# Kernel tuning notes

Hardware: AMD Instinct MI355X
Metric: run time of the kernel (lower is better)

The kernel has to match this reference:

```python
import jax, jax.numpy as jnp
import numpy as np
from jax import lax

ALPHA = 0.85
C1 = 0.01 ** 2
C2 = 0.03 ** 2


def _avg_pool3(x):
    # F.avg_pool2d(x, 3, 1, 1) with count_include_pad=True: zero-pad, divide by 9.
    s = lax.reduce_window(x, jnp.array(0.0, x.dtype), lax.add,
                          (1, 1, 3, 3), (1, 1, 1, 1),
                          [(0, 0), (0, 0), (1, 1), (1, 1)])
    return s / jnp.array(9.0, x.dtype)


def _ssim(x, y):
    mu_x = _avg_pool3(x)
    mu_y = _avg_pool3(y)
    sigma_x = jnp.clip(_avg_pool3(x * x) - mu_x * mu_x, 0.0, None)
    sigma_y = jnp.clip(_avg_pool3(y * y) - mu_y * mu_y, 0.0, None)
    sigma_xy = _avg_pool3(x * y) - mu_x * mu_y
    ssim_n = (2.0 * mu_x * mu_y + C1) * (2.0 * sigma_xy + C2)
    ssim_d = (mu_x * mu_x + mu_y * mu_y + C1) * (sigma_x + sigma_y + C2)
    return jnp.clip((1.0 - ssim_n / ssim_d) / 2.0, 0.0, 1.0)


def _warp_right(right_img, disp):
    # grid_sample(bilinear, border, align_corners=True) where y maps identically
    # to its own row -> a 1D horizontal bilinear gather at x_sample = x - disp.
    B, C, H, W = right_img.shape
    x_base = jnp.arange(W, dtype=disp.dtype).reshape(1, 1, 1, W)
    x_sample = x_base - disp                      # [B,1,H,W]
    xs = jnp.clip(x_sample, 0.0, W - 1.0)         # border padding
    x0 = jnp.floor(xs)
    w = xs - x0                                   # frac weight
    i0 = x0.astype(jnp.int32)
    i1 = jnp.minimum(i0 + 1, W - 1)
    i0b = jnp.broadcast_to(i0, (B, C, H, W))
    i1b = jnp.broadcast_to(i1, (B, C, H, W))
    g0 = jnp.take_along_axis(right_img, i0b, axis=3)
    g1 = jnp.take_along_axis(right_img, i1b, axis=3)
    warped = (1.0 - w) * g0 + w * g1              # w broadcasts over C
    valid = ((x_sample > 0) & (x_sample < W - 1)).astype(disp.dtype)
    return warped, valid


def setup_inputs() -> dict:
    key = jax.random.key(0)
    k1, k2, k3 = jax.random.split(key, 3)
    B, H, W = 8, 720, 1280
    disp = jax.random.normal(k1, (B, 1, H, W), dtype=jnp.float32)
    left_img = jax.random.uniform(k2, (B, 3, H, W), dtype=jnp.float32)
    right_img = jax.random.uniform(k3, (B, 3, H, W), dtype=jnp.float32)
    return {"disp": disp, "left_img": left_img, "right_img": right_img}


def reference(disp, left_img, right_img):
    right_warped, valid = _warp_right(right_img, disp)
    l1_err = jnp.mean(jnp.abs(left_img - right_warped), axis=1, keepdims=True)
    ssim_err = jnp.mean(_ssim(left_img, right_warped), axis=1, keepdims=True)
    photo_err = ALPHA * ssim_err + (1.0 - ALPHA) * l1_err
    n_valid = jnp.maximum(jnp.sum(valid), 1.0)
    return jnp.sum(photo_err * valid) / n_valid
```

## Files before the change

### kernel.cpp

```cpp
#include <hip/hip_runtime.h>


#define P_ALPHA 0.85f
#define P_C1 1e-4f
#define P_C2 9e-4f

constexpr int COLS = 62;
constexpr int RPW  = 18;
constexpr int WAVES = 4;

__global__ __launch_bounds__(256)
void photo_loss_kernel(const float* __restrict__ disp,
                       const float* __restrict__ left,
                       const float* __restrict__ right,
                       float* __restrict__ acc,
                       int H, int W)
{
    __shared__ float redpv[WAVES];
    __shared__ float redv[WAVES];

    const int tid  = threadIdx.x;
    const int lane = tid & 63;
    const int w    = tid >> 6;
    const int b    = blockIdx.z;
    const int col  = blockIdx.x * COLS + lane - 1;
    const int rowStart = (blockIdx.y * WAVES + w) * RPW;

    const int planeHW = H * W;
    const float* __restrict__ dispb = disp  + b * planeHW;
    const float* __restrict__ L0 = left  + (b * 3 + 0) * planeHW;
    const float* __restrict__ L1 = left  + (b * 3 + 1) * planeHW;
    const float* __restrict__ L2 = left  + (b * 3 + 2) * planeHW;
    const float* __restrict__ R0 = right + (b * 3 + 0) * planeHW;
    const float* __restrict__ R1 = right + (b * 3 + 1) * planeHW;
    const float* __restrict__ R2 = right + (b * 3 + 2) * planeHW;

    const float wm1f = (float)(W - 1);
    const bool col_in  = (col >= 0) && (col < W);
    const bool out_col = (lane >= 1) && (lane <= COLS) && (col < W);

    float rsx[3][3], rsy[3][3], rsxx[3][3], rsyy[3][3], rsxy[3][3];
    float l1r[3], vr[3];

    float sum_pv = 0.f, sum_v = 0.f;

    auto step_load = [&](int r, int s) {
        float x0 = 0.f, x1 = 0.f, x2 = 0.f;
        float y0 = 0.f, y1 = 0.f, y2 = 0.f;
        float valid = 0.f;
        if (col_in && (unsigned)r < (unsigned)H) {
            const int off = r * W + col;
            const float d = dispb[off];
            x0 = L0[off]; x1 = L1[off]; x2 = L2[off];
            const float xs = (float)col - d;
            valid = (xs > 0.f && xs < wm1f) ? 1.f : 0.f;
            float xc = fminf(fmaxf(xs, 0.f), wm1f);
            float xf = floorf(xc);
            float fr = xc - xf;
            int i0 = (int)xf;
            int i1 = min(i0 + 1, W - 1);
            const int ro = r * W;
            float g00 = R0[ro + i0], g01 = R0[ro + i1];
            float g10 = R1[ro + i0], g11 = R1[ro + i1];
            float g20 = R2[ro + i0], g21 = R2[ro + i1];
            const float omf = 1.f - fr;
            y0 = omf * g00 + fr * g01;
            y1 = omf * g10 + fr * g11;
            y2 = omf * g20 + fr * g21;
        }
        float xl, xr, yl, yr;
        xl = __shfl_up(x0, 1, 64); xr = __shfl_down(x0, 1, 64);
        yl = __shfl_up(y0, 1, 64); yr = __shfl_down(y0, 1, 64);
        rsx[0][s]  = xl + x0 + xr;
        rsy[0][s]  = yl + y0 + yr;
        rsxx[0][s] = xl * xl + x0 * x0 + xr * xr;
        rsyy[0][s] = yl * yl + y0 * y0 + yr * yr;
        rsxy[0][s] = xl * yl + x0 * y0 + xr * yr;

        xl = __shfl_up(x1, 1, 64); xr = __shfl_down(x1, 1, 64);
        yl = __shfl_up(y1, 1, 64); yr = __shfl_down(y1, 1, 64);
        rsx[1][s]  = xl + x1 + xr;
        rsy[1][s]  = yl + y1 + yr;
        rsxx[1][s] = xl * xl + x1 * x1 + xr * xr;
        rsyy[1][s] = yl * yl + y1 * y1 + yr * yr;
        rsxy[1][s] = xl * yl + x1 * y1 + xr * yr;

        xl = __shfl_up(x2, 1, 64); xr = __shfl_down(x2, 1, 64);
        yl = __shfl_up(y2, 1, 64); yr = __shfl_down(y2, 1, 64);
        rsx[2][s]  = xl + x2 + xr;
        rsy[2][s]  = yl + y2 + yr;
        rsxx[2][s] = xl * xl + x2 * x2 + xr * xr;
        rsyy[2][s] = yl * yl + y2 * y2 + yr * yr;
        rsxy[2][s] = xl * yl + x2 * y2 + xr * yr;

        l1r[s] = fabsf(x0 - y0) + fabsf(x1 - y1) + fabsf(x2 - y2);
        vr[s]  = valid;
    };

    auto emit = [&](int cs) {
        float ssim_sum = 0.f;
        #pragma unroll
        for (int c = 0; c < 3; ++c) {
            const float inv9 = 1.f / 9.f;
            float mu_x = (rsx[c][0]  + rsx[c][1]  + rsx[c][2])  * inv9;
            float mu_y = (rsy[c][0]  + rsy[c][1]  + rsy[c][2])  * inv9;
            float exx  = (rsxx[c][0] + rsxx[c][1] + rsxx[c][2]) * inv9;
            float eyy  = (rsyy[c][0] + rsyy[c][1] + rsyy[c][2]) * inv9;
            float exy  = (rsxy[c][0] + rsxy[c][1] + rsxy[c][2]) * inv9;
            float sig_x  = fmaxf(exx - mu_x * mu_x, 0.f);
            float sig_y  = fmaxf(eyy - mu_y * mu_y, 0.f);
            float sig_xy = exy - mu_x * mu_y;
            float n  = (2.f * mu_x * mu_y + P_C1) * (2.f * sig_xy + P_C2);
            float dd = (mu_x * mu_x + mu_y * mu_y + P_C1) * (sig_x + sig_y + P_C2);
            float s  = (1.f - n * __builtin_amdgcn_rcpf(dd)) * 0.5f;
            s = fminf(fmaxf(s, 0.f), 1.f);
            ssim_sum += s;
        }
        float photo = P_ALPHA * (ssim_sum * (1.f / 3.f))
                    + (1.f - P_ALPHA) * (l1r[cs] * (1.f / 3.f));
        if (out_col) {
            sum_pv += photo * vr[cs];
            sum_v  += vr[cs];
        }
    };

    step_load(rowStart - 1, 0);
    step_load(rowStart,     1);

    int r = rowStart + 1;
    for (int jo = 0; jo < RPW / 3; ++jo) {
        step_load(r,     2); emit(1);
        step_load(r + 1, 0); emit(2);
        step_load(r + 2, 1); emit(0);
        r += 3;
    }

    #pragma unroll
    for (int off = 32; off > 0; off >>= 1) {
        sum_pv += __shfl_down(sum_pv, off, 64);
        sum_v  += __shfl_down(sum_v,  off, 64);
    }
    if (lane == 0) { redpv[w] = sum_pv; redv[w] = sum_v; }
    __syncthreads();
    if (tid == 0) {
        atomicAdd(&acc[0], redpv[0] + redpv[1] + redpv[2] + redpv[3]);
        atomicAdd(&acc[1], redv[0]  + redv[1]  + redv[2]  + redv[3]);
    }
}

__global__ void photo_loss_finalize(const float* __restrict__ acc,
                                    float* __restrict__ out)
{
    out[0] = acc[0] / fmaxf(acc[1], 1.f);
}

extern "C" void kernel_launch(void* const* d_in, const int* in_sizes, int n_in,
                              void* d_out, int out_size, void* d_ws, size_t ws_size,
                              hipStream_t stream)
{
    const float* disp  = (const float*)d_in[0];
    const float* left  = (const float*)d_in[1];
    const float* right = (const float*)d_in[2];
    float* out = (float*)d_out;
    float* acc = (float*)d_ws;

    const int B = 8, H = 720, W = 1280;

    hipMemsetAsync(acc, 0, 2 * sizeof(float), stream);

    dim3 grid((W + COLS - 1) / COLS, H / (WAVES * RPW), B);
    dim3 block(256);
    photo_loss_kernel<<<grid, block, 0, stream>>>(disp, left, right, acc, H, W);
    photo_loss_finalize<<<1, 1, 0, stream>>>(acc, out);
}
```

Measured before the change: 263.7 us.

## Prefetch next row's disparity and left pixels, make loads branchless, shrink RPW

The row loop is fully unrolled and software-pipelined: the disparity and left-image values for row r+1 are loaded while row r's dependent right-image gathers and the SSIM emit are being computed. The per-row bounds branch is replaced by clamped indices and multiplicative masks, so every lane always issues its loads. Rows per wave drop from 18 to 12, which gives more blocks for latency hiding but raises the fraction of re-read halo rows and adds more atomics. Full unrolling may also raise register pressure.

```diff
diff --git a/kernel.cpp b/kernel.cpp
--- a/kernel.cpp
+++ b/kernel.cpp
@@ -5,8 +5,8 @@
 #define P_C1 1e-4f
 #define P_C2 9e-4f
 
-constexpr int COLS = 62;
-constexpr int RPW  = 18;
+constexpr int COLS  = 62;
+constexpr int RPW   = 12;
 constexpr int WAVES = 4;
 
 __global__ __launch_bounds__(256)
@@ -36,72 +36,20 @@
     const float* __restrict__ R2 = right + (b * 3 + 2) * planeHW;
 
     const float wm1f = (float)(W - 1);
-    const bool col_in  = (col >= 0) && (col < W);
-    const bool out_col = (lane >= 1) && (lane <= COLS) && (col < W);
+    const int   colC = min(max(col, 0), W - 1);
+    const float colv = (col >= 0 && col < W) ? 1.f : 0.f;
+    const float ocm  = (lane >= 1 && lane <= COLS && col < W) ? 1.f : 0.f;
 
     float rsx[3][3], rsy[3][3], rsxx[3][3], rsyy[3][3], rsxy[3][3];
     float l1r[3], vr[3];
 
     float sum_pv = 0.f, sum_v = 0.f;
 
-    auto step_load = [&](int r, int s) {
-        float x0 = 0.f, x1 = 0.f, x2 = 0.f;
-        float y0 = 0.f, y1 = 0.f, y2 = 0.f;
-        float valid = 0.f;
-        if (col_in && (unsigned)r < (unsigned)H) {
-            const int off = r * W + col;
-            const float d = dispb[off];
-            x0 = L0[off]; x1 = L1[off]; x2 = L2[off];
-            const float xs = (float)col - d;
-            valid = (xs > 0.f && xs < wm1f) ? 1.f : 0.f;
-            float xc = fminf(fmaxf(xs, 0.f), wm1f);
-            float xf = floorf(xc);
-            float fr = xc - xf;
-            int i0 = (int)xf;
-            int i1 = min(i0 + 1, W - 1);
-            const int ro = r * W;
-            float g00 = R0[ro + i0], g01 = R0[ro + i1];
-            float g10 = R1[ro + i0], g11 = R1[ro + i1];
-            float g20 = R2[ro + i0], g21 = R2[ro + i1];
-            const float omf = 1.f - fr;
-            y0 = omf * g00 + fr * g01;
-            y1 = omf * g10 + fr * g11;
-            y2 = omf * g20 + fr * g21;
-        }
-        float xl, xr, yl, yr;
-        xl = __shfl_up(x0, 1, 64); xr = __shfl_down(x0, 1, 64);
-        yl = __shfl_up(y0, 1, 64); yr = __shfl_down(y0, 1, 64);
-        rsx[0][s]  = xl + x0 + xr;
-        rsy[0][s]  = yl + y0 + yr;
-        rsxx[0][s] = xl * xl + x0 * x0 + xr * xr;
-        rsyy[0][s] = yl * yl + y0 * y0 + yr * yr;
-        rsxy[0][s] = xl * yl + x0 * y0 + xr * yr;
-
-        xl = __shfl_up(x1, 1, 64); xr = __shfl_down(x1, 1, 64);
-        yl = __shfl_up(y1, 1, 64); yr = __shfl_down(y1, 1, 64);
-        rsx[1][s]  = xl + x1 + xr;
-        rsy[1][s]  = yl + y1 + yr;
-        rsxx[1][s] = xl * xl + x1 * x1 + xr * xr;
-        rsyy[1][s] = yl * yl + y1 * y1 + yr * yr;
-        rsxy[1][s] = xl * yl + x1 * y1 + xr * yr;
-
-        xl = __shfl_up(x2, 1, 64); xr = __shfl_down(x2, 1, 64);
-        yl = __shfl_up(y2, 1, 64); yr = __shfl_down(y2, 1, 64);
-        rsx[2][s]  = xl + x2 + xr;
-        rsy[2][s]  = yl + y2 + yr;
-        rsxx[2][s] = xl * xl + x2 * x2 + xr * xr;
-        rsyy[2][s] = yl * yl + y2 * y2 + yr * yr;
-        rsxy[2][s] = xl * yl + x2 * y2 + xr * yr;
-
-        l1r[s] = fabsf(x0 - y0) + fabsf(x1 - y1) + fabsf(x2 - y2);
-        vr[s]  = valid;
-    };
-
     auto emit = [&](int cs) {
+        const float inv9 = 1.f / 9.f;
         float ssim_sum = 0.f;
         #pragma unroll
         for (int c = 0; c < 3; ++c) {
-            const float inv9 = 1.f / 9.f;
             float mu_x = (rsx[c][0]  + rsx[c][1]  + rsx[c][2])  * inv9;
             float mu_y = (rsy[c][0]  + rsy[c][1]  + rsy[c][2])  * inv9;
             float exx  = (rsxx[c][0] + rsxx[c][1] + rsxx[c][2]) * inv9;
@@ -118,21 +66,87 @@
         }
         float photo = P_ALPHA * (ssim_sum * (1.f / 3.f))
                     + (1.f - P_ALPHA) * (l1r[cs] * (1.f / 3.f));
-        if (out_col) {
-            sum_pv += photo * vr[cs];
-            sum_v  += vr[cs];
-        }
+        sum_pv += photo * vr[cs] * ocm;
+        sum_v  += vr[cs] * ocm;
     };
 
-    step_load(rowStart - 1, 0);
-    step_load(rowStart,     1);
+    float dC, xC0, xC1, xC2;
+    {
+        const int r  = rowStart - 1;
+        const int rc = min(max(r, 0), H - 1);
+        const int off = rc * W + colC;
+        dC = dispb[off]; xC0 = L0[off]; xC1 = L1[off]; xC2 = L2[off];
+    }
 
-    int r = rowStart + 1;
-    for (int jo = 0; jo < RPW / 3; ++jo) {
-        step_load(r,     2); emit(1);
-        step_load(r + 1, 0); emit(2);
-        step_load(r + 2, 1); emit(0);
-        r += 3;
+    #pragma unroll
+    for (int j = 0; j <= RPW + 2; ++j) {
+        const int s = j % 3;
+        const int r = rowStart - 1 + j;
+        if (j <= RPW + 1) {
+            const int   rc = min(max(r, 0), H - 1);
+            const float rv = (r >= 0 && r < H) ? 1.f : 0.f;
+            const float m  = rv * colv;
+
+            const float xs  = (float)col - dC;
+            const float xcl = fminf(fmaxf(xs, 0.f), wm1f);
+            const float xf  = floorf(xcl);
+            const float fr  = xcl - xf;
+            const int   i0  = (int)xf;
+            const int   i1  = min(i0 + 1, W - 1);
+            const int   ro  = rc * W;
+            const float g00 = R0[ro + i0], g01 = R0[ro + i1];
+            const float g10 = R1[ro + i0], g11 = R1[ro + i1];
+            const float g20 = R2[ro + i0], g21 = R2[ro + i1];
+
+            float dN = 0.f, xN0 = 0.f, xN1 = 0.f, xN2 = 0.f;
+            if (j <= RPW) {
+                const int rn   = min(max(r + 1, 0), H - 1);
+                const int offn = rn * W + colC;
+                dN = dispb[offn]; xN0 = L0[offn]; xN1 = L1[offn]; xN2 = L2[offn];
+            }
+
+            if (j >= 3) emit((s + 1) % 3);
+
+            const float omf = 1.f - fr;
+            const float y0 = (omf * g00 + fr * g01) * m;
+            const float y1 = (omf * g10 + fr * g11) * m;
+            const float y2 = (omf * g20 + fr * g21) * m;
+            const float x0 = xC0 * m;
+            const float x1 = xC1 * m;
+            const float x2 = xC2 * m;
+
+            float xl, xr, yl, yr;
+            xl = __shfl_up(x0, 1, 64); xr = __shfl_down(x0, 1, 64);
+            yl = __shfl_up(y0, 1, 64); yr = __shfl_down(y0, 1, 64);
+            rsx[0][s]  = xl + x0 + xr;
+            rsy[0][s]  = yl + y0 + yr;
+            rsxx[0][s] = xl * xl + x0 * x0 + xr * xr;
+            rsyy[0][s] = yl * yl + y0 * y0 + yr * yr;
+            rsxy[0][s] = xl * yl + x0 * y0 + xr * yr;
+
+            xl = __shfl_up(x1, 1, 64); xr = __shfl_down(x1, 1, 64);
+            yl = __shfl_up(y1, 1, 64); yr = __shfl_down(y1, 1, 64);
+            rsx[1][s]  = xl + x1 + xr;
+            rsy[1][s]  = yl + y1 + yr;
+            rsxx[1][s] = xl * xl + x1 * x1 + xr * xr;
+            rsyy[1][s] = yl * yl + y1 * y1 + yr * yr;
+            rsxy[1][s] = xl * yl + x1 * y1 + xr * yr;
+
+            xl = __shfl_up(x2, 1, 64); xr = __shfl_down(x2, 1, 64);
+            yl = __shfl_up(y2, 1, 64); yr = __shfl_down(y2, 1, 64);
+            rsx[2][s]  = xl + x2 + xr;
+            rsy[2][s]  = yl + y2 + yr;
+            rsxx[2][s] = xl * xl + x2 * x2 + xr * xr;
+            rsyy[2][s] = yl * yl + y2 * y2 + yr * yr;
+            rsxy[2][s] = xl * yl + x2 * y2 + xr * yr;
+
+            l1r[s] = fabsf(x0 - y0) + fabsf(x1 - y1) + fabsf(x2 - y2);
+            vr[s]  = (xs > 0.f && xs < wm1f) ? 1.f : 0.f;
+
+            dC = dN; xC0 = xN0; xC1 = xN1; xC2 = xN2;
+        } else {
+            emit((s + 1) % 3);
+        }
     }
 
     #pragma unroll
```

Result: faster. 242.2 us (-8.2%).
